# Optimization experiments

Hardware: AMD Instinct MI355X
Metric: run time of the kernel (lower is better)

Reference implementation:

```python
import jax, jax.numpy as jnp
import numpy as np

N, E = 10000, 160000
IN_C, HID, OUT_C = 128, 128, 64
LAYERS, HEADS = 3, 8
D_HEAD = HID // HEADS


def setup_inputs() -> dict:
    key = jax.random.key(0)
    ks = jax.random.split(key, 12)
    sc = lambda k, shape, fan: (jax.random.normal(k, shape, jnp.float32) / np.float32(np.sqrt(fan)))
    return dict(
        x=jax.random.normal(ks[0], (N, IN_C), jnp.float32),
        edge_index=jax.random.randint(ks[1], (2, E), 0, N, jnp.int32),
        W1=sc(ks[2], (IN_C, HID), IN_C), b1=jnp.zeros((HID,), jnp.float32),
        Wq=sc(ks[3], (LAYERS, HID, HID), HID), bq=jnp.zeros((LAYERS, HID), jnp.float32),
        Wk=sc(ks[4], (LAYERS, HID, HID), HID), bk=jnp.zeros((LAYERS, HID), jnp.float32),
        Wv=sc(ks[5], (LAYERS, HID, HID), HID), bv=jnp.zeros((LAYERS, HID), jnp.float32),
        W2=sc(ks[6], (HID, OUT_C), HID), b2=jnp.zeros((OUT_C,), jnp.float32),
    )


def reference(x, edge_index, W1, b1, Wq, bq, Wk, bk, Wv, bv, W2, b2):
    n = x.shape[0]
    # gcn_norm with self-loops (edge weights = 1)
    loops = jnp.arange(n, dtype=edge_index.dtype)
    src = jnp.concatenate([edge_index[0], loops])  # x_j source nodes
    dst = jnp.concatenate([edge_index[1], loops])  # x_i target nodes (aggregation)
    deg = jax.ops.segment_sum(jnp.ones_like(src, dtype=x.dtype), dst, num_segments=n)
    dinv = jnp.where(deg > 0, jax.lax.rsqrt(deg), jnp.zeros_like(deg))
    norm = dinv[src] * dinv[dst]  # [E+N]

    # dropout layers are identity in eval mode
    h = jax.nn.relu(x @ W1 + b1)
    x_all = h[:, None, :]  # [N, 1, C]

    scale = np.float32(1.0 / np.sqrt(D_HEAD))
    for l in range(LAYERS):
        L = x_all.shape[1]
        # project at node level (linear commutes with gather)
        q = (x_all[:, -1] @ Wq[l] + bq[l])[dst]              # [Et, C], query = last-layer target feats
        k = (x_all @ Wk[l] + bk[l])[src]                     # [Et, L, C], key = source history
        v = (x_all @ Wv[l] + bv[l])[src]                     # [Et, L, C]
        Et = q.shape[0]
        qh = q.reshape(Et, HEADS, D_HEAD)
        kh = k.reshape(Et, L, HEADS, D_HEAD)
        vh = v.reshape(Et, L, HEADS, D_HEAD)
        scores = jnp.einsum('ehd,elhd->ehl', qh, kh) * scale  # attention over history axis L
        attn = jax.nn.softmax(scores, axis=-1)                 # (attn dropout is identity in eval)
        msg = jnp.einsum('ehl,elhd->ehd', attn, vh).reshape(Et, HID)
        agg = jax.ops.segment_sum(norm[:, None] * msg, dst, num_segments=n)
        h_new = jax.nn.relu(agg)
        x_all = jnp.concatenate([x_all, h_new[:, None, :]], axis=1)

    logits = x_all[:, -1] @ W2 + b2
    return jax.nn.log_softmax(logits, axis=1)
```

## Files before the change

kernel.cpp:

```cpp
#include <hip/hip_runtime.h>
#include <hip/hip_fp16.h>
#include <math.h>

#define NN 10000
#define EE 160000
#define HID 128
constexpr int N128 = NN * HID;
constexpr int PSTR = 768;
constexpr int HOFF = 384;

typedef _Float16 f16;
typedef f16 half8 __attribute__((ext_vector_type(8)));
typedef f16 f16x2 __attribute__((ext_vector_type(2)));
typedef float f32x4 __attribute__((ext_vector_type(4)));

#if __has_builtin(__builtin_amdgcn_fdot2)
__device__ inline float fdot2(f16x2 a, f16x2 b, float c) { return __builtin_amdgcn_fdot2(a, b, c, false); }
#else
__device__ inline float fdot2(f16x2 a, f16x2 b, float c) {
    return fmaf((float)a[0], (float)b[0], fmaf((float)a[1], (float)b[1], c));
}
#endif

__global__ __launch_bounds__(256) void cnt_count(const int* __restrict__ dst, int* __restrict__ cnt) {
    int e = blockIdx.x * 256 + threadIdx.x;
    if (e < EE) atomicAdd(&cnt[dst[e]], 1);
}

__global__ __launch_bounds__(256) void scan_rowptr(const int* __restrict__ cnt, int* __restrict__ rowptr,
                                                   float* __restrict__ dinv) {
    __shared__ int part[256];
    const int PER = (NN + 255) / 256;
    int t = threadIdx.x;
    int base = t * PER;
    int sum = 0;
    for (int i = 0; i < PER; ++i) {
        int idx = base + i;
        if (idx < NN) {
            int c = cnt[idx];
            sum += c;
            dinv[idx] = rsqrtf((float)c + 1.0f);
        }
    }
    part[t] = sum;
    __syncthreads();
    for (int ofs = 1; ofs < 256; ofs <<= 1) {
        int v = (t >= ofs) ? part[t - ofs] : 0;
        __syncthreads();
        part[t] += v;
        __syncthreads();
    }
    int run = (t > 0) ? part[t - 1] : 0;
    for (int i = 0; i < PER; ++i) {
        int idx = base + i;
        if (idx <= NN) rowptr[idx] = run;
        if (idx < NN) run += cnt[idx];
    }
}

__global__ __launch_bounds__(256) void scatter_edges(const int* __restrict__ ei,
                                                     const int* __restrict__ rowptr,
                                                     int* __restrict__ fill,
                                                     int* __restrict__ esorted) {
    int e = blockIdx.x * 256 + threadIdx.x;
    if (e < EE) {
        int s = ei[e], d = ei[EE + e];
        int pos = rowptr[d] + atomicAdd(&fill[d], 1);
        esorted[pos] = s;
    }
}

__global__ __launch_bounds__(256) void prep_fused(const float* __restrict__ W1, const float* __restrict__ Wq,
                                                  const float* __restrict__ Wk, const float* __restrict__ Wv,
                                                  const float* __restrict__ W2, f16* __restrict__ Wt,
                                                  int4* __restrict__ zbuf) {
    int b = blockIdx.x;
    int t = threadIdx.x;
    if (b >= 11) {
        zbuf[(b - 11) * 256 + t] = make_int4(0, 0, 0, 0);
        return;
    }
    f16* dst = Wt + (size_t)b * 16384;
    if (b == 10) {
        int oc = t & 63, k0 = (t >> 6) * 32;
        for (int kk = 0; kk < 32; ++kk) {
            int k = k0 + kk;
            dst[oc * 128 + k] = (f16)W2[(size_t)k * 64 + oc];
        }
        return;
    }
    const float* src = (b == 0) ? W1
                     : (b < 4)  ? Wq + (size_t)(b - 1) * 16384
                     : (b < 7)  ? Wk + (size_t)(b - 4) * 16384
                                : Wv + (size_t)(b - 7) * 16384;
    int oc = t >> 1;
    int k0 = (t & 1) * 64;
    for (int kk = 0; kk < 64; ++kk) {
        int k = k0 + kk;
        dst[oc * 128 + k] = (f16)src[k * 128 + oc];
    }
}

struct GJob {
    const void* in; const f16* Wt; const float* bias; const float* rowscale;
    void* out; int ldi; int ldo; int mode; int inF32;
    const f16* Wt2; const float* bias2;
};
struct GJobs { GJob j[7]; };

__global__ __launch_bounds__(256) void gemm_mfma(GJobs jobs, int nrows) {
    const GJob jb = jobs.j[blockIdx.y];
    __shared__ f16 Xl[64 * 128];
    __shared__ f16 Wl[128 * 128];
    const int t = threadIdx.x;
    const int row0 = blockIdx.x * 64;

    half8 zero8;
#pragma unroll
    for (int z = 0; z < 8; ++z) zero8[z] = (f16)0.f;

#pragma unroll
    for (int it = 0; it < 4; ++it) {
        int idx = t + it * 256;
        int r = idx >> 4, c = idx & 15;
        int gr = row0 + r;
        half8 v = zero8;
        if (gr < nrows) {
            if (jb.inF32) {
                const float* fin = (const float*)jb.in + (size_t)gr * jb.ldi + c * 8;
                float4 f0 = ((const float4*)fin)[0];
                float4 f1 = ((const float4*)fin)[1];
                v[0] = (f16)f0.x; v[1] = (f16)f0.y; v[2] = (f16)f0.z; v[3] = (f16)f0.w;
                v[4] = (f16)f1.x; v[5] = (f16)f1.y; v[6] = (f16)f1.z; v[7] = (f16)f1.w;
            } else {
                v = *(const half8*)((const f16*)jb.in + (size_t)gr * jb.ldi + c * 8);
            }
        }
        *(half8*)((char*)Xl + r * 256 + ((c * 16) ^ ((r & 7) << 4))) = v;
    }
#pragma unroll
    for (int it = 0; it < 8; ++it) {
        int idx = t + it * 256;
        int r = idx >> 4, c = idx & 15;
        half8 v = *(const half8*)(jb.Wt + (size_t)r * 128 + c * 8);
        *(half8*)((char*)Wl + r * 256 + ((c * 16) ^ ((r & 7) << 4))) = v;
    }
    __syncthreads();

    const int w = t >> 6, l = t & 63;
    const int lr = l & 15;
    const int lk = l >> 4;

    f32x4 acc[8];
#pragma unroll
    for (int tn = 0; tn < 8; ++tn)
#pragma unroll
        for (int i = 0; i < 4; ++i) acc[tn][i] = 0.f;

    const int arow = w * 16 + lr;
    const int axor = (arow & 7) << 4;
    const int bxor = (lr & 7) << 4;

#pragma unroll
    for (int ks = 0; ks < 4; ++ks) {
        int koff = (ks * 4 + lk) * 16;
        half8 a = *(const half8*)((const char*)Xl + arow * 256 + (koff ^ axor));
#pragma unroll
        for (int tn = 0; tn < 8; ++tn) {
            int oc = tn * 16 + lr;
            half8 b = *(const half8*)((const char*)Wl + oc * 256 + (koff ^ bxor));
            acc[tn] = __builtin_amdgcn_mfma_f32_16x16x32_f16(a, b, acc[tn], 0, 0, 0);
        }
    }

    const int rbase = row0 + w * 16 + (lk << 2);
    float brs[4];
#pragma unroll
    for (int i = 0; i < 4; ++i)
        brs[i] = jb.rowscale ? ((rbase + i < nrows) ? jb.rowscale[rbase + i] : 0.f) : 1.0f;
    float bsv[8];
#pragma unroll
    for (int tn = 0; tn < 8; ++tn) bsv[tn] = jb.bias[tn * 16 + lr];

    if (jb.mode == 0) {
        float* op = (float*)jb.out;
#pragma unroll
        for (int tn = 0; tn < 8; ++tn)
#pragma unroll
            for (int i = 0; i < 4; ++i) {
                int gr = rbase + i;
                if (gr < nrows) op[(size_t)gr * jb.ldo + tn * 16 + lr] = acc[tn][i] + brs[i] * bsv[tn];
            }
    } else if (jb.mode == 1) {
        f16* op = (f16*)jb.out;
#pragma unroll
        for (int tn = 0; tn < 8; ++tn)
#pragma unroll
            for (int i = 0; i < 4; ++i) {
                int gr = rbase + i;
                if (gr < nrows) op[(size_t)gr * jb.ldo + tn * 16 + lr] = (f16)fmaxf(acc[tn][i] + brs[i] * bsv[tn], 0.f);
            }
    } else if (jb.mode == 2) {
        f16* op = (f16*)jb.out;
#pragma unroll
        for (int tn = 0; tn < 8; ++tn)
#pragma unroll
            for (int i = 0; i < 4; ++i) {
                int gr = rbase + i;
                if (gr < nrows) op[(size_t)gr * jb.ldo + tn * 16 + lr] = (f16)(acc[tn][i] + brs[i] * bsv[tn]);
            }
    } else {
        __syncthreads();
#pragma unroll
        for (int tn = 0; tn < 8; ++tn)
#pragma unroll
            for (int i = 0; i < 4; ++i) {
                f16 v = (f16)fmaxf(acc[tn][i] + brs[i] * bsv[tn], 0.f);
                int lrow = w * 16 + (lk << 2) + i;
                int col = tn * 16 + lr;
                int byte = lrow * 256 + ((((col >> 3) * 16) ^ ((lrow & 7) << 4))) + (col & 7) * 2;
                *(f16*)((char*)Xl + byte) = v;
            }
#pragma unroll
        for (int it = 0; it < 4; ++it) {
            int idx = t + it * 256;
            int r = idx >> 4, c = idx & 15;
            half8 v = *(const half8*)(jb.Wt2 + (size_t)r * 128 + c * 8);
            *(half8*)((char*)Wl + r * 256 + ((c * 16) ^ ((r & 7) << 4))) = v;
        }
        __syncthreads();

        f32x4 acc2[4];
#pragma unroll
        for (int tn = 0; tn < 4; ++tn)
#pragma unroll
            for (int i = 0; i < 4; ++i) acc2[tn][i] = 0.f;
#pragma unroll
        for (int ks = 0; ks < 4; ++ks) {
            int koff = (ks * 4 + lk) * 16;
            half8 a = *(const half8*)((const char*)Xl + arow * 256 + (koff ^ axor));
#pragma unroll
            for (int tn = 0; tn < 4; ++tn) {
                int oc = tn * 16 + lr;
                half8 b = *(const half8*)((const char*)Wl + oc * 256 + (koff ^ bxor));
                acc2[tn] = __builtin_amdgcn_mfma_f32_16x16x32_f16(a, b, acc2[tn], 0, 0, 0);
            }
        }
        float bs2[4];
#pragma unroll
        for (int tn = 0; tn < 4; ++tn) bs2[tn] = jb.bias2[tn * 16 + lr];
#pragma unroll
        for (int i = 0; i < 4; ++i) {
            float lg[4];
#pragma unroll
            for (int tn = 0; tn < 4; ++tn) lg[tn] = acc2[tn][i] + bs2[tn];
            float m = fmaxf(fmaxf(lg[0], lg[1]), fmaxf(lg[2], lg[3]));
#pragma unroll
            for (int sft = 1; sft <= 8; sft <<= 1) m = fmaxf(m, __shfl_xor(m, sft));
            float den = 0.f;
#pragma unroll
            for (int tn = 0; tn < 4; ++tn) den += __expf(lg[tn] - m);
#pragma unroll
            for (int sft = 1; sft <= 8; sft <<= 1) den += __shfl_xor(den, sft);
            float lden = logf(den);
            int gr = rbase + i;
            if (gr < nrows) {
                float* op = (float*)jb.out + (size_t)gr * jb.ldo;
#pragma unroll
                for (int tn = 0; tn < 4; ++tn) op[tn * 16 + lr] = lg[tn] - m - lden;
            }
        }
    }
}

__global__ __launch_bounds__(256) void sgather5(
    const int* __restrict__ rowptr, const int* __restrict__ esorted,
    const float* __restrict__ dinv,
    const f16* __restrict__ hsrc , f16* __restrict__ Sh, float* __restrict__ srow) {
    int d = (blockIdx.x * 256 + threadIdx.x) >> 6;
    int lam = threadIdx.x & 63;
    int qe = lam >> 4, le = lam & 15;
    if (d >= NN) return;
    int i0 = rowptr[d], nE = rowptr[d + 1] - i0 + 1;
    float dvd = dinv[d];
    float u[8];
#pragma unroll
    for (int i = 0; i < 8; ++i) u[i] = 0.f;
    float ssum = 0.f;

    auto ldb = [&](int b, float& w, half8& h) {
        int j = b + qe;
        int s = (j < nE - 1) ? esorted[i0 + j] : d;
        w = (j < nE) ? dinv[s] : 0.f;
        h = *(const half8*)(hsrc + (size_t)s * PSTR + le * 8);
    };
    auto cmp = [&](float w, const half8& h) {
#pragma unroll
        for (int i = 0; i < 8; ++i) u[i] = fmaf(w, (float)h[i], u[i]);
        ssum += w;
    };

    float wA, wB; half8 hA, hB;
    ldb(0, wA, hA);
    for (int b = 0; b < nE; b += 8) {
        ldb(b + 4, wB, hB);
        cmp(wA, hA);
        ldb(b + 8, wA, hA);
        cmp(wB, hB);
    }
#pragma unroll
    for (int i = 0; i < 8; ++i) {
        u[i] += __shfl_xor(u[i], 16);
        u[i] += __shfl_xor(u[i], 32);
    }
    ssum += __shfl_xor(ssum, 16);
    ssum += __shfl_xor(ssum, 32);
    if (qe == 0) {
        half8 o;
#pragma unroll
        for (int i = 0; i < 8; ++i) o[i] = (f16)(dvd * u[i]);
        *(half8*)(Sh + (size_t)d * 128 + le * 8) = o;
        if (le == 0) srow[d] = dvd * ssum;
    }
}

template<int L>
__global__ __launch_bounds__(256) void node_attn5(
    const int* __restrict__ rowptr, const int* __restrict__ esorted,
    const float* __restrict__ dinv,
    const f16* __restrict__ qh, const f16* __restrict__ pack,
    f16* __restrict__ uh) {
    int d = (blockIdx.x * 256 + threadIdx.x) >> 6;
    int lam = threadIdx.x & 63;
    int qe = lam >> 4, le = lam & 15;
    if (d >= NN) return;
    int i0 = rowptr[d], nE = rowptr[d + 1] - i0 + 1;
    float dvd = dinv[d];
    half8 q8 = *(const half8*)(qh + (size_t)d * 128 + le * 8);
    const f16x2* qp = (const f16x2*)&q8;
    float u[8];
#pragma unroll
    for (int i = 0; i < 8; ++i) u[i] = 0.f;

    auto ldb = [&](int b, float& w, half8 (&k)[L], half8 (&h)[L]) {
        int j = b + qe;
        int s = (j < nE - 1) ? esorted[i0 + j] : d;
        w = (j < nE) ? dinv[s] : 0.f;
        const f16* bp = pack + (size_t)s * PSTR + le * 8;
#pragma unroll
        for (int l = 0; l < L; ++l) {
            k[l] = *(const half8*)(bp + l * 128);
            h[l] = *(const half8*)(bp + HOFF + l * 128);
        }
    };
    auto cmp = [&](float w, const half8 (&k)[L], const half8 (&h)[L]) {
        float sc[L];
#pragma unroll
        for (int l = 0; l < L; ++l) {
            const f16x2* kp = (const f16x2*)&k[l];
            float p = 0.f;
#pragma unroll
            for (int i = 0; i < 4; ++i) p = fdot2(qp[i], kp[i], p);
            p += __shfl_xor(p, 1);
            sc[l] = p * 0.25f;
        }
        float m = sc[0];
#pragma unroll
        for (int l = 1; l < L; ++l) m = fmaxf(m, sc[l]);
        float den = 0.f;
#pragma unroll
        for (int l = 0; l < L; ++l) { sc[l] = __expf(sc[l] - m); den += sc[l]; }
        float wg = w * __builtin_amdgcn_rcpf(den);
#pragma unroll
        for (int l = 0; l < L; ++l) {
            float a = sc[l] * wg;
#pragma unroll
            for (int i = 0; i < 8; ++i) u[i] = fmaf(a, (float)h[l][i], u[i]);
        }
    };

    float wA, wB; half8 kA[L], hA[L], kB[L], hB[L];
    ldb(0, wA, kA, hA);
    for (int b = 0; b < nE; b += 8) {
        ldb(b + 4, wB, kB, hB);
        cmp(wA, kA, hA);
        ldb(b + 8, wA, kA, hA);
        cmp(wB, kB, hB);
    }
#pragma unroll
    for (int i = 0; i < 8; ++i) {
        u[i] += __shfl_xor(u[i], 16);
        u[i] += __shfl_xor(u[i], 32);
    }
    if (qe == 0) {
        half8 o;
#pragma unroll
        for (int i = 0; i < 8; ++i) o[i] = (f16)(dvd * u[i]);
        *(half8*)(uh + (size_t)d * 128 + le * 8) = o;
    }
}

extern "C" void kernel_launch(void* const* d_in, const int* in_sizes, int n_in,
                              void* d_out, int out_size, void* d_ws, size_t ws_size,
                              hipStream_t stream) {
    (void)in_sizes; (void)n_in; (void)out_size; (void)ws_size;
    const float* x  = (const float*)d_in[0];
    const int*   ei = (const int*)d_in[1];
    const float* W1 = (const float*)d_in[2];
    const float* b1 = (const float*)d_in[3];
    const float* Wq = (const float*)d_in[4];
    const float* bq = (const float*)d_in[5];
    const float* Wk = (const float*)d_in[6];
    const float* bk = (const float*)d_in[7];
    const float* Wv = (const float*)d_in[8];
    const float* bv = (const float*)d_in[9];
    const float* W2 = (const float*)d_in[10];
    const float* b2 = (const float*)d_in[11];
    float* out = (float*)d_out;

    int*    cnt     = (int*)d_ws;
    int*    fill    = cnt + 16384;
    int*    rowptr  = fill + 16384;
    int*    esorted = rowptr + 16384;
    float*  dinv    = (float*)(esorted + 163840);
    float*  srow    = dinv + 16384;
    f16*    pack    = (f16*)(srow + 16384);
    f16*    Sh      = pack + (size_t)NN * PSTR;
    f16*    qh      = Sh + N128;
    f16*    uh      = qh + N128;
    f16*    Wt      = uh + N128;

    prep_fused<<<43, 256, 0, stream>>>(W1, Wq, Wk, Wv, W2, Wt, (int4*)cnt);
    cnt_count<<<(EE + 255) / 256, 256, 0, stream>>>(ei + EE, cnt);
    scan_rowptr<<<1, 256, 0, stream>>>(cnt, rowptr, dinv);
    scatter_edges<<<(EE + 255) / 256, 256, 0, stream>>>(ei, rowptr, fill, esorted);

    const int gx = (NN + 63) / 64;
    auto WT = [&](int m) { return Wt + (size_t)m * 16384; };
    auto H  = [&](int lev) { return pack + HOFF + lev * 128; };
    auto K  = [&](int lev) { return pack + lev * 128; };

    {
        GJobs jobs{};
        jobs.j[0] = {x, WT(0), b1, nullptr, H(0), HID, PSTR, 1, 1, nullptr, nullptr};
        gemm_mfma<<<dim3(gx, 1), 256, 0, stream>>>(jobs, NN);
    }

    const int nblocks = (NN * 64 + 255) / 256;

    sgather5<<<nblocks, 256, 0, stream>>>(rowptr, esorted, dinv, pack + HOFF, Sh, srow);
    {
        GJobs jobs{};
        jobs.j[0] = {Sh, WT(7), bv, srow, H(1), HID, PSTR, 1, 0, nullptr, nullptr};
        gemm_mfma<<<dim3(gx, 1), 256, 0, stream>>>(jobs, NN);
    }

    for (int l = 1; l < 3; ++l) {
        int L = l + 1;
        GJobs jobs{};
        jobs.j[0] = {H(L - 1), WT(1 + l), bq + l * HID, nullptr, qh, PSTR, HID, 2, 0, nullptr, nullptr};
        for (int lev = 0; lev < L; ++lev)
            jobs.j[1 + lev] = {H(lev), WT(4 + l), bk + l * HID, nullptr, K(lev), PSTR, PSTR, 2, 0, nullptr, nullptr};
        gemm_mfma<<<dim3(gx, 1 + L), 256, 0, stream>>>(jobs, NN);

        if (L == 2) node_attn5<2><<<nblocks, 256, 0, stream>>>(rowptr, esorted, dinv, qh, pack, uh);
        if (L == 3) node_attn5<3><<<nblocks, 256, 0, stream>>>(rowptr, esorted, dinv, qh, pack, uh);

        GJobs vjob{};
        if (L == 2) {
            vjob.j[0] = {uh, WT(7 + l), bv + l * HID, srow, H(2), HID, PSTR, 1, 0, nullptr, nullptr};
        } else {
            vjob.j[0] = {uh, WT(7 + l), bv + l * HID, srow, out, HID, 64, 3, 0, WT(10), b2};
        }
        gemm_mfma<<<dim3(gx, 1), 256, 0, stream>>>(vjob, NN);
    }
}
```

Baseline: 169.0 us.

## Split single-job GEMMs into column halves and merge edge counting into weight prep

New measurement: 175.6 us. +3.9%, slower.

```diff
diff --git a/kernel.cpp b/kernel.cpp
--- a/kernel.cpp
+++ b/kernel.cpp
@@ -22,13 +22,44 @@
 }
 #endif
 
-__global__ __launch_bounds__(256) void cnt_count(const int* __restrict__ dst, int* __restrict__ cnt) {
-    int e = blockIdx.x * 256 + threadIdx.x;
-    if (e < EE) atomicAdd(&cnt[dst[e]], 1);
+__global__ __launch_bounds__(256) void zero_cnt(int4* __restrict__ p) {
+    p[blockIdx.x * 256 + threadIdx.x] = make_int4(0, 0, 0, 0);
+}
+
+__global__ __launch_bounds__(256) void prep_cnt(const float* __restrict__ W1, const float* __restrict__ Wq,
+                                                const float* __restrict__ Wk, const float* __restrict__ Wv,
+                                                const float* __restrict__ W2, f16* __restrict__ Wt,
+                                                const int* __restrict__ dst, int* __restrict__ cnt) {
+    int b = blockIdx.x;
+    int t = threadIdx.x;
+    if (b >= 11) {
+        int e = (b - 11) * 256 + t;
+        if (e < EE) atomicAdd(&cnt[dst[e]], 1);
+        return;
+    }
+    f16* dstw = Wt + (size_t)b * 16384;
+    if (b == 10) {
+        int oc = t & 63, k0 = (t >> 6) * 32;
+        for (int kk = 0; kk < 32; ++kk) {
+            int k = k0 + kk;
+            dstw[oc * 128 + k] = (f16)W2[(size_t)k * 64 + oc];
+        }
+        return;
+    }
+    const float* src = (b == 0) ? W1
+                     : (b < 4)  ? Wq + (size_t)(b - 1) * 16384
+                     : (b < 7)  ? Wk + (size_t)(b - 4) * 16384
+                                : Wv + (size_t)(b - 7) * 16384;
+    int oc = t >> 1;
+    int k0 = (t & 1) * 64;
+    for (int kk = 0; kk < 64; ++kk) {
+        int k = k0 + kk;
+        dstw[oc * 128 + k] = (f16)src[k * 128 + oc];
+    }
 }
 
 __global__ __launch_bounds__(256) void scan_rowptr(const int* __restrict__ cnt, int* __restrict__ rowptr,
-                                                   float* __restrict__ dinv) {
+                                                   int* __restrict__ rowfill, float* __restrict__ dinv) {
     __shared__ int part[256];
     const int PER = (NN + 255) / 256;
     int t = threadIdx.x;
@@ -54,50 +85,18 @@
     for (int i = 0; i < PER; ++i) {
         int idx = base + i;
         if (idx <= NN) rowptr[idx] = run;
-        if (idx < NN) run += cnt[idx];
+        if (idx < NN) { rowfill[idx] = run; run += cnt[idx]; }
     }
 }
 
 __global__ __launch_bounds__(256) void scatter_edges(const int* __restrict__ ei,
-                                                     const int* __restrict__ rowptr,
-                                                     int* __restrict__ fill,
+                                                     int* __restrict__ rowfill,
                                                      int* __restrict__ esorted) {
     int e = blockIdx.x * 256 + threadIdx.x;
     if (e < EE) {
         int s = ei[e], d = ei[EE + e];
-        int pos = rowptr[d] + atomicAdd(&fill[d], 1);
+        int pos = atomicAdd(&rowfill[d], 1);
         esorted[pos] = s;
-    }
-}
-
-__global__ __launch_bounds__(256) void prep_fused(const float* __restrict__ W1, const float* __restrict__ Wq,
-                                                  const float* __restrict__ Wk, const float* __restrict__ Wv,
-                                                  const float* __restrict__ W2, f16* __restrict__ Wt,
-                                                  int4* __restrict__ zbuf) {
-    int b = blockIdx.x;
-    int t = threadIdx.x;
-    if (b >= 11) {
-        zbuf[(b - 11) * 256 + t] = make_int4(0, 0, 0, 0);
-        return;
-    }
-    f16* dst = Wt + (size_t)b * 16384;
-    if (b == 10) {
-        int oc = t & 63, k0 = (t >> 6) * 32;
-        for (int kk = 0; kk < 32; ++kk) {
-            int k = k0 + kk;
-            dst[oc * 128 + k] = (f16)W2[(size_t)k * 64 + oc];
-        }
-        return;
-    }
-    const float* src = (b == 0) ? W1
-                     : (b < 4)  ? Wq + (size_t)(b - 1) * 16384
-                     : (b < 7)  ? Wk + (size_t)(b - 4) * 16384
-                                : Wv + (size_t)(b - 7) * 16384;
-    int oc = t >> 1;
-    int k0 = (t & 1) * 64;
-    for (int kk = 0; kk < 64; ++kk) {
-        int k = k0 + kk;
-        dst[oc * 128 + k] = (f16)src[k * 128 + oc];
     }
 }
 
@@ -108,10 +107,11 @@
 };
 struct GJobs { GJob j[7]; };
 
+template<int NTN>
 __global__ __launch_bounds__(256) void gemm_mfma(GJobs jobs, int nrows) {
     const GJob jb = jobs.j[blockIdx.y];
     __shared__ f16 Xl[64 * 128];
-    __shared__ f16 Wl[128 * 128];
+    __shared__ f16 Wl[NTN * 16 * 128];
     const int t = threadIdx.x;
     const int row0 = blockIdx.x * 64;
 
@@ -139,7 +139,7 @@
         *(half8*)((char*)Xl + r * 256 + ((c * 16) ^ ((r & 7) << 4))) = v;
     }
 #pragma unroll
-    for (int it = 0; it < 8; ++it) {
+    for (int it = 0; it < NTN; ++it) {
         int idx = t + it * 256;
         int r = idx >> 4, c = idx & 15;
         half8 v = *(const half8*)(jb.Wt + (size_t)r * 128 + c * 8);
@@ -151,9 +151,9 @@
     const int lr = l & 15;
     const int lk = l >> 4;
 
-    f32x4 acc[8];
-#pragma unroll
-    for (int tn = 0; tn < 8; ++tn)
+    f32x4 acc[NTN];
+#pragma unroll
+    for (int tn = 0; tn < NTN; ++tn)
 #pragma unroll
         for (int i = 0; i < 4; ++i) acc[tn][i] = 0.f;
 
@@ -166,7 +166,7 @@
         int koff = (ks * 4 + lk) * 16;
         half8 a = *(const half8*)((const char*)Xl + arow * 256 + (koff ^ axor));
 #pragma unroll
-        for (int tn = 0; tn < 8; ++tn) {
+        for (int tn = 0; tn < NTN; ++tn) {
             int oc = tn * 16 + lr;
             half8 b = *(const half8*)((const char*)Wl + oc * 256 + (koff ^ bxor));
             acc[tn] = __builtin_amdgcn_mfma_f32_16x16x32_f16(a, b, acc[tn], 0, 0, 0);
@@ -178,14 +178,14 @@
 #pragma unroll
     for (int i = 0; i < 4; ++i)
         brs[i] = jb.rowscale ? ((rbase + i < nrows) ? jb.rowscale[rbase + i] : 0.f) : 1.0f;
-    float bsv[8];
-#pragma unroll
-    for (int tn = 0; tn < 8; ++tn) bsv[tn] = jb.bias[tn * 16 + lr];
+    float bsv[NTN];
+#pragma unroll
+    for (int tn = 0; tn < NTN; ++tn) bsv[tn] = jb.bias[tn * 16 + lr];
 
     if (jb.mode == 0) {
         float* op = (float*)jb.out;
 #pragma unroll
-        for (int tn = 0; tn < 8; ++tn)
+        for (int tn = 0; tn < NTN; ++tn)
 #pragma unroll
             for (int i = 0; i < 4; ++i) {
                 int gr = rbase + i;
@@ -194,7 +194,7 @@
     } else if (jb.mode == 1) {
         f16* op = (f16*)jb.out;
 #pragma unroll
-        for (int tn = 0; tn < 8; ++tn)
+        for (int tn = 0; tn < NTN; ++tn)
 #pragma unroll
             for (int i = 0; i < 4; ++i) {
                 int gr = rbase + i;
@@ -203,13 +203,13 @@
     } else if (jb.mode == 2) {
         f16* op = (f16*)jb.out;
 #pragma unroll
-        for (int tn = 0; tn < 8; ++tn)
+        for (int tn = 0; tn < NTN; ++tn)
 #pragma unroll
             for (int i = 0; i < 4; ++i) {
                 int gr = rbase + i;
                 if (gr < nrows) op[(size_t)gr * jb.ldo + tn * 16 + lr] = (f16)(acc[tn][i] + brs[i] * bsv[tn]);
             }
-    } else {
+    } else if constexpr (NTN == 8) {
         __syncthreads();
 #pragma unroll
         for (int tn = 0; tn < 8; ++tn)
@@ -419,8 +419,8 @@
     float* out = (float*)d_out;
 
     int*    cnt     = (int*)d_ws;
-    int*    fill    = cnt + 16384;
-    int*    rowptr  = fill + 16384;
+    int*    rowfill = cnt + 16384;
+    int*    rowptr  = rowfill + 16384;
     int*    esorted = rowptr + 16384;
     float*  dinv    = (float*)(esorted + 163840);
     float*  srow    = dinv + 16384;
@@ -430,10 +430,10 @@
     f16*    uh      = qh + N128;
     f16*    Wt      = uh + N128;
 
-    prep_fused<<<43, 256, 0, stream>>>(W1, Wq, Wk, Wv, W2, Wt, (int4*)cnt);
-    cnt_count<<<(EE + 255) / 256, 256, 0, stream>>>(ei + EE, cnt);
-    scan_rowptr<<<1, 256, 0, stream>>>(cnt, rowptr, dinv);
-    scatter_edges<<<(EE + 255) / 256, 256, 0, stream>>>(ei, rowptr, fill, esorted);
+    zero_cnt<<<16, 256, 0, stream>>>((int4*)cnt);
+    prep_cnt<<<11 + (EE + 255) / 256, 256, 0, stream>>>(W1, Wq, Wk, Wv, W2, Wt, ei + EE, cnt);
+    scan_rowptr<<<1, 256, 0, stream>>>(cnt, rowptr, rowfill, dinv);
+    scatter_edges<<<(EE + 255) / 256, 256, 0, stream>>>(ei, rowfill, esorted);
 
     const int gx = (NN + 63) / 64;
     auto WT = [&](int m) { return Wt + (size_t)m * 16384; };
@@ -442,8 +442,9 @@
 
     {
         GJobs jobs{};
-        jobs.j[0] = {x, WT(0), b1, nullptr, H(0), HID, PSTR, 1, 1, nullptr, nullptr};
-        gemm_mfma<<<dim3(gx, 1), 256, 0, stream>>>(jobs, NN);
+        jobs.j[0] = {x, WT(0),            b1,      nullptr, H(0),      HID, PSTR, 1, 1, nullptr, nullptr};
+        jobs.j[1] = {x, WT(0) + 64 * 128, b1 + 64, nullptr, H(0) + 64, HID, PSTR, 1, 1, nullptr, nullptr};
+        gemm_mfma<4><<<dim3(gx, 2), 256, 0, stream>>>(jobs, NN);
     }
 
     const int nblocks = (NN * 64 + 255) / 256;
@@ -451,8 +452,9 @@
     sgather5<<<nblocks, 256, 0, stream>>>(rowptr, esorted, dinv, pack + HOFF, Sh, srow);
     {
         GJobs jobs{};
-        jobs.j[0] = {Sh, WT(7), bv, srow, H(1), HID, PSTR, 1, 0, nullptr, nullptr};
-        gemm_mfma<<<dim3(gx, 1), 256, 0, stream>>>(jobs, NN);
+        jobs.j[0] = {Sh, WT(7),            bv,      srow, H(1),      HID, PSTR, 1, 0, nullptr, nullptr};
+        jobs.j[1] = {Sh, WT(7) + 64 * 128, bv + 64, srow, H(1) + 64, HID, PSTR, 1, 0, nullptr, nullptr};
+        gemm_mfma<4><<<dim3(gx, 2), 256, 0, stream>>>(jobs, NN);
     }
 
     for (int l = 1; l < 3; ++l) {
@@ -461,17 +463,20 @@
         jobs.j[0] = {H(L - 1), WT(1 + l), bq + l * HID, nullptr, qh, PSTR, HID, 2, 0, nullptr, nullptr};
         for (int lev = 0; lev < L; ++lev)
             jobs.j[1 + lev] = {H(lev), WT(4 + l), bk + l * HID, nullptr, K(lev), PSTR, PSTR, 2, 0, nullptr, nullptr};
-        gemm_mfma<<<dim3(gx, 1 + L), 256, 0, stream>>>(jobs, NN);
+        gemm_mfma<8><<<dim3(gx, 1 + L), 256, 0, stream>>>(jobs, NN);
 
         if (L == 2) node_attn5<2><<<nblocks, 256, 0, stream>>>(rowptr, esorted, dinv, qh, pack, uh);
         if (L == 3) node_attn5<3><<<nblocks, 256, 0, stream>>>(rowptr, esorted, dinv, qh, pack, uh);
 
-        GJobs vjob{};
         if (L == 2) {
-            vjob.j[0] = {uh, WT(7 + l), bv + l * HID, srow, H(2), HID, PSTR, 1, 0, nullptr, nullptr};
+            GJobs vjob{};
+            vjob.j[0] = {uh, WT(8),            bv + HID,      srow, H(2),      HID, PSTR, 1, 0, nullptr, nullptr};
+            vjob.j[1] = {uh, WT(8) + 64 * 128, bv + HID + 64, srow, H(2) + 64, HID, PSTR, 1, 0, nullptr, nullptr};
+            gemm_mfma<4><<<dim3(gx, 2), 256, 0, stream>>>(vjob, NN);
         } else {
-            vjob.j[0] = {uh, WT(7 + l), bv + l * HID, srow, out, HID, 64, 3, 0, WT(10), b2};
-        }
-        gemm_mfma<<<dim3(gx, 1), 256, 0, stream>>>(vjob, NN);
-    }
-}
+            GJobs vjob{};
+            vjob.j[0] = {uh, WT(9), bv + 2 * HID, srow, out, HID, 64, 3, 0, WT(10), b2};
+            gemm_mfma<8><<<dim3(gx, 1), 256, 0, stream>>>(vjob, NN);
+        }
+    }
+}
```
